# Kernel tuning notes

Measured on AMD Instinct MI355X. Metric: run time of the kernel, lower is better.

Reference implementation:

```python
import jax, jax.numpy as jnp
import numpy as np

B, H, S, D = 4, 8, 8192, 64


def setup_inputs() -> dict:
    key = jax.random.key(0)
    kq, kk, kv_, kqm, kkm = jax.random.split(key, 5)
    q = jax.random.normal(kq, (B, H, S, D), dtype=jnp.float32)
    k = jax.random.normal(kk, (B, H, S, D), dtype=jnp.float32)
    v = jax.random.normal(kv_, (B, H, S, D), dtype=jnp.float32)
    q_mask = jax.random.randint(kqm, (B, S), 0, 2).astype(jnp.bool_)
    kv_mask = jax.random.randint(kkm, (B, S), 0, 2).astype(jnp.bool_)
    return {"q": q, "k": k, "v": v, "q_mask": q_mask, "kv_mask": kv_mask}


def reference(q, k, v, q_mask, kv_mask):
    # Linear (kernelized) attention branch: feature map phi(x) = elu(x) + 1
    qe = jax.nn.elu(q) + 1.0
    ke = jax.nn.elu(k) + 1.0
    qm = q_mask.astype(q.dtype)[:, None, :, None]   # [B,1,S,1]
    km = kv_mask.astype(q.dtype)[:, None, :, None]
    qe = qe * qm
    ke = ke * km
    ve = v * km
    s = v.shape[2]
    # kv: [B,H,D,D] contraction over kv sequence
    kv = jnp.einsum('bhsd,bhsc->bhdc', ke, ve / s)
    # normalizer per query position: [B,H,L]
    div = 1.0 / (jnp.einsum('bhld,bhsd->bhl', qe, ke) + 1e-6)
    out = s * jnp.einsum('bhld,bhdc,bhl->bhlc', qe, kv, div)
    return out
```

## Files before the change

kernel.cpp:

```cpp
#include <hip/hip_runtime.h>


#define S_LEN 8192
#define NBH 32
#define KVSTRIDE 4160

typedef __attribute__((ext_vector_type(4))) float f32x4;

__device__ __forceinline__ float elu1(float x) {
  return x > 0.0f ? (x + 1.0f) : __expf(x);
}

__global__ __launch_bounds__(256) void k1_partial(
    const float* __restrict__ kin, const float* __restrict__ vin,
    const int* __restrict__ kv_mask, float* __restrict__ partials, int seg_rows) {
  __shared__ float ke_lds[64 * 64];
  __shared__ float ve_lds[64 * 64];
  const int tid = threadIdx.x;
  const int seg = blockIdx.x, bh = blockIdx.y, b = bh >> 3;
  const int rbase = seg * seg_rows;
  const int dg = tid >> 4, cg = tid & 15;
  const float* kbase = kin + (size_t)bh * S_LEN * 64;
  const float* vbase = vin + (size_t)bh * S_LEN * 64;
  const int* mbase = kv_mask + b * S_LEN;

  f32x4 ka[4], va[4], kb[4], vb[4];
  float ma[4], mb[4];
  float acc[4][4];
#pragma unroll
  for (int i = 0; i < 4; ++i)
#pragma unroll
    for (int j = 0; j < 4; ++j) acc[i][j] = 0.f;
  f32x4 ksump = {0.f, 0.f, 0.f, 0.f};

#define LOAD_T(K, V, M, r0_)                                           \
  {                                                                    \
    const float* kp_ = kbase + (size_t)(r0_) * 64;                     \
    const float* vp_ = vbase + (size_t)(r0_) * 64;                     \
    _Pragma("unroll")                                                  \
    for (int i_ = 0; i_ < 4; ++i_) {                                   \
      int f_ = tid + 256 * i_;                                         \
      K[i_] = *(const f32x4*)(kp_ + (size_t)f_ * 4);                   \
      V[i_] = *(const f32x4*)(vp_ + (size_t)f_ * 4);                   \
      M[i_] = mbase[(r0_) + (tid >> 4) + 16 * i_] ? 1.0f : 0.0f;       \
    }                                                                  \
  }

#define STORE_T(K, V, M)                                               \
  {                                                                    \
    _Pragma("unroll")                                                  \
    for (int i_ = 0; i_ < 4; ++i_) {                                   \
      int row_ = (tid >> 4) + 16 * i_;                                 \
      int c4_ = (tid & 15) * 4;                                        \
      float m_ = M[i_];                                                \
      float mv_ = m_ * (1.0f / 8192.0f);                               \
      f32x4 ke4_, ve4_;                                                \
      _Pragma("unroll")                                                \
      for (int j_ = 0; j_ < 4; ++j_) {                                 \
        ke4_[j_] = elu1(K[i_][j_]) * m_;                               \
        ve4_[j_] = V[i_][j_] * mv_;                                    \
      }                                                                \
      ksump += ke4_;      \
      *(f32x4*)&ke_lds[row_ * 64 + c4_] = ke4_;                        \
      *(f32x4*)&ve_lds[row_ * 64 + c4_] = ve4_;                        \
    }                                                                  \
  }

#define COMPUTE_T()                                                    \
  {                                                                    \
    _Pragma("unroll 4")                                                \
    for (int s_ = 0; s_ < 64; ++s_) {                                  \
      f32x4 kd_ = *(const f32x4*)&ke_lds[s_ * 64 + dg * 4];            \
      f32x4 vc_ = *(const f32x4*)&ve_lds[s_ * 64 + cg * 4];            \
      _Pragma("unroll")                                                \
      for (int i_ = 0; i_ < 4; ++i_)                                   \
        _Pragma("unroll")                                              \
        for (int j_ = 0; j_ < 4; ++j_)                                 \
          acc[i_][j_] = fmaf(kd_[i_], vc_[j_], acc[i_][j_]);           \
    }                                                                  \
  }

  const int ntiles = seg_rows >> 6;
  LOAD_T(ka, va, ma, rbase)
  for (int t = 0; t < ntiles; t += 2) {
    if (t) __syncthreads();
    STORE_T(ka, va, ma)
    LOAD_T(kb, vb, mb, rbase + (t + 1) * 64)
    __syncthreads();
    COMPUTE_T()
    __syncthreads();
    STORE_T(kb, vb, mb)
    if (t + 2 < ntiles) LOAD_T(ka, va, ma, rbase + (t + 2) * 64)
    __syncthreads();
    COMPUTE_T()
  }

  float* p = partials + ((size_t)bh * gridDim.x + seg) * KVSTRIDE;
#pragma unroll
  for (int i = 0; i < 4; ++i) {
    f32x4 o;
#pragma unroll
    for (int j = 0; j < 4; ++j) o[j] = acc[i][j];
    *(f32x4*)&p[(dg * 4 + i) * 64 + cg * 4] = o;
  }
  __syncthreads();
  *(f32x4*)&ke_lds[tid * 4] = ksump;
  __syncthreads();
  if (tid < 64) {
    float s = 0.f;
#pragma unroll
    for (int g = 0; g < 16; ++g)
      s += ke_lds[(g * 16 + (tid >> 2)) * 4 + (tid & 3)];
    p[4096 + tid] = s;
  }
#undef LOAD_T
#undef STORE_T
#undef COMPUTE_T
}

__global__ __launch_bounds__(256) void k2_reduce(
    const float* __restrict__ partials, float* __restrict__ kvg, int nchunk) {
  const int idx = blockIdx.x * 256 + threadIdx.x;
  if (idx >= NBH * KVSTRIDE) return;
  const int bh = idx / KVSTRIDE;
  const int e = idx - bh * KVSTRIDE;
  const float* p = partials + (size_t)bh * nchunk * KVSTRIDE + e;
  float s0 = 0.f, s1 = 0.f, s2 = 0.f, s3 = 0.f;
  int c = 0;
  for (; c + 4 <= nchunk; c += 4) {
    s0 += p[(size_t)(c + 0) * KVSTRIDE];
    s1 += p[(size_t)(c + 1) * KVSTRIDE];
    s2 += p[(size_t)(c + 2) * KVSTRIDE];
    s3 += p[(size_t)(c + 3) * KVSTRIDE];
  }
  for (; c < nchunk; ++c) s0 += p[(size_t)c * KVSTRIDE];
  kvg[idx] = (s0 + s1) + (s2 + s3);
}

__global__ __launch_bounds__(256) void k3_out(
    const float* __restrict__ qin, const int* __restrict__ q_mask,
    const float* __restrict__ kvg, float* __restrict__ out) {
  __shared__ float qe_lds[64 * 66];
  __shared__ float kv_lds[64 * 64];
  __shared__ float den_lds[256 * 4];
  __shared__ float inv_lds[64];
  const int tid = threadIdx.x;
  const int rb = blockIdx.x, bh = blockIdx.y, b = bh >> 3;
  const int r0 = rb * 64;
  const int lg = tid >> 4, cg = tid & 15;
  const float* kvb = kvg + (size_t)bh * KVSTRIDE;
  const f32x4 ks4 = *(const f32x4*)(kvb + 4096 + cg * 4);
  const float* qb = qin + ((size_t)bh * S_LEN + r0) * 64;

  f32x4 denp;
#pragma unroll
  for (int i = 0; i < 4; ++i) {
    int f = tid + 256 * i;
    int row = (tid >> 4) + 16 * i, c4 = cg * 4;
    float m = q_mask[b * S_LEN + r0 + row] ? 1.0f : 0.0f;
    f32x4 qw = *(const f32x4*)(qb + (size_t)f * 4);
    f32x4 qe;
#pragma unroll
    for (int j = 0; j < 4; ++j) qe[j] = elu1(qw[j]) * m;
    *(f32x4*)&qe_lds[row * 66 + c4] = qe;
    denp[i] = qe[0] * ks4[0] + qe[1] * ks4[1] + qe[2] * ks4[2] + qe[3] * ks4[3];
    *(f32x4*)&kv_lds[f * 4] = *(const f32x4*)(kvb + (size_t)f * 4);
  }
  *(f32x4*)&den_lds[tid * 4] = denp;
  __syncthreads();
  if (tid < 64) {
    float s = 0.f;
#pragma unroll
    for (int g = 0; g < 16; ++g)
      s += den_lds[((tid & 15) * 16 + g) * 4 + (tid >> 4)];
    inv_lds[tid] = 8192.0f / (s + 1e-6f);
  }

  float acc[4][4];
#pragma unroll
  for (int i = 0; i < 4; ++i)
#pragma unroll
    for (int j = 0; j < 4; ++j) acc[i][j] = 0.f;

#pragma unroll 8
  for (int d = 0; d < 64; d += 2) {
    float2 qv0 = *(const float2*)&qe_lds[(lg * 4 + 0) * 66 + d];
    float2 qv1 = *(const float2*)&qe_lds[(lg * 4 + 1) * 66 + d];
    float2 qv2 = *(const float2*)&qe_lds[(lg * 4 + 2) * 66 + d];
    float2 qv3 = *(const float2*)&qe_lds[(lg * 4 + 3) * 66 + d];
    f32x4 kv0 = *(const f32x4*)&kv_lds[d * 64 + cg * 4];
    f32x4 kv1 = *(const f32x4*)&kv_lds[(d + 1) * 64 + cg * 4];
#pragma unroll
    for (int j = 0; j < 4; ++j) {
      acc[0][j] = fmaf(qv0.x, kv0[j], fmaf(qv0.y, kv1[j], acc[0][j]));
      acc[1][j] = fmaf(qv1.x, kv0[j], fmaf(qv1.y, kv1[j], acc[1][j]));
      acc[2][j] = fmaf(qv2.x, kv0[j], fmaf(qv2.y, kv1[j], acc[2][j]));
      acc[3][j] = fmaf(qv3.x, kv0[j], fmaf(qv3.y, kv1[j], acc[3][j]));
    }
  }
  __syncthreads();
#pragma unroll
  for (int il = 0; il < 4; ++il) {
    int row = lg * 4 + il;
    float inv = inv_lds[row];
    f32x4 o;
#pragma unroll
    for (int j = 0; j < 4; ++j) o[j] = acc[il][j] * inv;
    *(f32x4*)(out + ((size_t)bh * S_LEN + r0 + row) * 64 + cg * 4) = o;
  }
}

extern "C" void kernel_launch(void* const* d_in, const int* in_sizes, int n_in,
                              void* d_out, int out_size, void* d_ws, size_t ws_size,
                              hipStream_t stream) {
  const float* q = (const float*)d_in[0];
  const float* k = (const float*)d_in[1];
  const float* v = (const float*)d_in[2];
  const int* qm = (const int*)d_in[3];
  const int* km = (const int*)d_in[4];
  float* out = (float*)d_out;

  int nchunk = 64;
  while (nchunk > 1) {
    size_t need = (size_t)NBH * nchunk * KVSTRIDE * 4 + (size_t)NBH * KVSTRIDE * 4;
    if (need <= ws_size) break;
    nchunk >>= 1;
  }
  float* partials = (float*)d_ws;
  float* kvg = partials + (size_t)NBH * nchunk * KVSTRIDE;
  int seg_rows = S_LEN / nchunk;

  k1_partial<<<dim3(nchunk, NBH), 256, 0, stream>>>(k, v, km, partials, seg_rows);
  int n_elem = NBH * KVSTRIDE;
  k2_reduce<<<dim3((n_elem + 255) / 256), 256, 0, stream>>>(partials, kvg, nchunk);
  k3_out<<<dim3(S_LEN / 64, NBH), 256, 0, stream>>>(q, qm, kvg, out);
}
```

Before: 242.9 us.

## Double-buffer LDS tiles in k1/k3, make k3 persistent, reduce chunk count

k1 now keeps two LDS buffers, so each iteration has a single barrier and the next tile's global load overlaps the current tile's FMA loop. k3 becomes a persistent kernel: each block loads kv once and walks 8 row tiles with a double-buffered qe tile. The denominator is computed inside the main d-loop instead of through a separate LDS reduction. Fewer chunks in k1 (16 instead of 64) shrink the partials traffic and k2's work. The cost is less parallelism in k1 (512 blocks) and k3 (512 blocks), which may leave CUs underfilled on a large GPU.

```diff
diff --git a/kernel.cpp b/kernel.cpp
--- a/kernel.cpp
+++ b/kernel.cpp
@@ -4,6 +4,8 @@
 #define S_LEN 8192
 #define NBH 32
 #define KVSTRIDE 4160
+#define NCHUNK 16
+#define K3_XB 16
 
 typedef __attribute__((ext_vector_type(4))) float f32x4;
 
@@ -14,8 +16,8 @@
 __global__ __launch_bounds__(256) void k1_partial(
     const float* __restrict__ kin, const float* __restrict__ vin,
     const int* __restrict__ kv_mask, float* __restrict__ partials, int seg_rows) {
-  __shared__ float ke_lds[64 * 64];
-  __shared__ float ve_lds[64 * 64];
+  __shared__ float ke_lds[2][64 * 64];
+  __shared__ float ve_lds[2][64 * 64];
   const int tid = threadIdx.x;
   const int seg = blockIdx.x, bh = blockIdx.y, b = bh >> 3;
   const int rbase = seg * seg_rows;
@@ -24,8 +26,8 @@
   const float* vbase = vin + (size_t)bh * S_LEN * 64;
   const int* mbase = kv_mask + b * S_LEN;
 
-  f32x4 ka[4], va[4], kb[4], vb[4];
-  float ma[4], mb[4];
+  f32x4 kr[4], vr[4];
+  float mr[4];
   float acc[4][4];
 #pragma unroll
   for (int i = 0; i < 4; ++i)
@@ -33,45 +35,44 @@
     for (int j = 0; j < 4; ++j) acc[i][j] = 0.f;
   f32x4 ksump = {0.f, 0.f, 0.f, 0.f};
 
-#define LOAD_T(K, V, M, r0_)                                           \
+#define LOAD_T(r0_)                                                    \
   {                                                                    \
     const float* kp_ = kbase + (size_t)(r0_) * 64;                     \
     const float* vp_ = vbase + (size_t)(r0_) * 64;                     \
     _Pragma("unroll")                                                  \
     for (int i_ = 0; i_ < 4; ++i_) {                                   \
       int f_ = tid + 256 * i_;                                         \
-      K[i_] = *(const f32x4*)(kp_ + (size_t)f_ * 4);                   \
-      V[i_] = *(const f32x4*)(vp_ + (size_t)f_ * 4);                   \
-      M[i_] = mbase[(r0_) + (tid >> 4) + 16 * i_] ? 1.0f : 0.0f;       \
-    }                                                                  \
-  }
-
-#define STORE_T(K, V, M)                                               \
-  {                                                                    \
-    _Pragma("unroll")                                                  \
-    for (int i_ = 0; i_ < 4; ++i_) {                                   \
-      int row_ = (tid >> 4) + 16 * i_;                                 \
-      int c4_ = (tid & 15) * 4;                                        \
-      float m_ = M[i_];                                                \
+      kr[i_] = *(const f32x4*)(kp_ + (size_t)f_ * 4);                  \
+      vr[i_] = *(const f32x4*)(vp_ + (size_t)f_ * 4);                  \
+      mr[i_] = mbase[(r0_) + dg + 16 * i_] ? 1.0f : 0.0f;              \
+    }                                                                  \
+  }
+
+#define STORE_T(buf_)                                                  \
+  {                                                                    \
+    _Pragma("unroll")                                                  \
+    for (int i_ = 0; i_ < 4; ++i_) {                                   \
+      int row_ = dg + 16 * i_;                                         \
+      float m_ = mr[i_];                                               \
       float mv_ = m_ * (1.0f / 8192.0f);                               \
       f32x4 ke4_, ve4_;                                                \
       _Pragma("unroll")                                                \
       for (int j_ = 0; j_ < 4; ++j_) {                                 \
-        ke4_[j_] = elu1(K[i_][j_]) * m_;                               \
-        ve4_[j_] = V[i_][j_] * mv_;                                    \
+        ke4_[j_] = elu1(kr[i_][j_]) * m_;                              \
+        ve4_[j_] = vr[i_][j_] * mv_;                                   \
       }                                                                \
-      ksump += ke4_;      \
-      *(f32x4*)&ke_lds[row_ * 64 + c4_] = ke4_;                        \
-      *(f32x4*)&ve_lds[row_ * 64 + c4_] = ve4_;                        \
-    }                                                                  \
-  }
-
-#define COMPUTE_T()                                                    \
+      ksump += ke4_;                                                   \
+      *(f32x4*)&ke_lds[buf_][row_ * 64 + cg * 4] = ke4_;               \
+      *(f32x4*)&ve_lds[buf_][row_ * 64 + cg * 4] = ve4_;               \
+    }                                                                  \
+  }
+
+#define COMPUTE_T(buf_)                                                \
   {                                                                    \
     _Pragma("unroll 4")                                                \
     for (int s_ = 0; s_ < 64; ++s_) {                                  \
-      f32x4 kd_ = *(const f32x4*)&ke_lds[s_ * 64 + dg * 4];            \
-      f32x4 vc_ = *(const f32x4*)&ve_lds[s_ * 64 + cg * 4];            \
+      f32x4 kd_ = *(const f32x4*)&ke_lds[buf_][s_ * 64 + dg * 4];      \
+      f32x4 vc_ = *(const f32x4*)&ve_lds[buf_][s_ * 64 + cg * 4];      \
       _Pragma("unroll")                                                \
       for (int i_ = 0; i_ < 4; ++i_)                                   \
         _Pragma("unroll")                                              \
@@ -81,18 +82,13 @@
   }
 
   const int ntiles = seg_rows >> 6;
-  LOAD_T(ka, va, ma, rbase)
-  for (int t = 0; t < ntiles; t += 2) {
-    if (t) __syncthreads();
-    STORE_T(ka, va, ma)
-    LOAD_T(kb, vb, mb, rbase + (t + 1) * 64)
+  LOAD_T(rbase)
+  STORE_T(0)
+  for (int t = 0; t < ntiles; ++t) {
     __syncthreads();
-    COMPUTE_T()
-    __syncthreads();
-    STORE_T(kb, vb, mb)
-    if (t + 2 < ntiles) LOAD_T(ka, va, ma, rbase + (t + 2) * 64)
-    __syncthreads();
-    COMPUTE_T()
+    if (t + 1 < ntiles) LOAD_T(rbase + (t + 1) * 64)
+    COMPUTE_T(t & 1)
+    if (t + 1 < ntiles) STORE_T((t + 1) & 1)
   }
 
   float* p = partials + ((size_t)bh * gridDim.x + seg) * KVSTRIDE;
@@ -104,13 +100,13 @@
     *(f32x4*)&p[(dg * 4 + i) * 64 + cg * 4] = o;
   }
   __syncthreads();
-  *(f32x4*)&ke_lds[tid * 4] = ksump;
+  *(f32x4*)&ke_lds[0][tid * 4] = ksump;
   __syncthreads();
   if (tid < 64) {
     float s = 0.f;
 #pragma unroll
     for (int g = 0; g < 16; ++g)
-      s += ke_lds[(g * 16 + (tid >> 2)) * 4 + (tid & 3)];
+      s += ke_lds[0][(g * 16 + (tid >> 2)) * 4 + (tid & 3)];
     p[4096 + tid] = s;
   }
 #undef LOAD_T
@@ -140,74 +136,93 @@
 __global__ __launch_bounds__(256) void k3_out(
     const float* __restrict__ qin, const int* __restrict__ q_mask,
     const float* __restrict__ kvg, float* __restrict__ out) {
-  __shared__ float qe_lds[64 * 66];
   __shared__ float kv_lds[64 * 64];
-  __shared__ float den_lds[256 * 4];
-  __shared__ float inv_lds[64];
+  __shared__ float qe_lds[2][64 * 68];
+  __shared__ float ks_lds[64];
   const int tid = threadIdx.x;
-  const int rb = blockIdx.x, bh = blockIdx.y, b = bh >> 3;
-  const int r0 = rb * 64;
+  const int xb = blockIdx.x, bh = blockIdx.y, b = bh >> 3;
   const int lg = tid >> 4, cg = tid & 15;
   const float* kvb = kvg + (size_t)bh * KVSTRIDE;
-  const f32x4 ks4 = *(const f32x4*)(kvb + 4096 + cg * 4);
-  const float* qb = qin + ((size_t)bh * S_LEN + r0) * 64;
-
-  f32x4 denp;
+  const float* qb = qin + (size_t)bh * S_LEN * 64;
+  const int* mb = q_mask + b * S_LEN;
+
 #pragma unroll
   for (int i = 0; i < 4; ++i) {
     int f = tid + 256 * i;
-    int row = (tid >> 4) + 16 * i, c4 = cg * 4;
-    float m = q_mask[b * S_LEN + r0 + row] ? 1.0f : 0.0f;
-    f32x4 qw = *(const f32x4*)(qb + (size_t)f * 4);
-    f32x4 qe;
-#pragma unroll
-    for (int j = 0; j < 4; ++j) qe[j] = elu1(qw[j]) * m;
-    *(f32x4*)&qe_lds[row * 66 + c4] = qe;
-    denp[i] = qe[0] * ks4[0] + qe[1] * ks4[1] + qe[2] * ks4[2] + qe[3] * ks4[3];
     *(f32x4*)&kv_lds[f * 4] = *(const f32x4*)(kvb + (size_t)f * 4);
   }
-  *(f32x4*)&den_lds[tid * 4] = denp;
-  __syncthreads();
-  if (tid < 64) {
-    float s = 0.f;
-#pragma unroll
-    for (int g = 0; g < 16; ++g)
-      s += den_lds[((tid & 15) * 16 + g) * 4 + (tid >> 4)];
-    inv_lds[tid] = 8192.0f / (s + 1e-6f);
-  }
-
-  float acc[4][4];
-#pragma unroll
-  for (int i = 0; i < 4; ++i)
-#pragma unroll
-    for (int j = 0; j < 4; ++j) acc[i][j] = 0.f;
-
+  if (tid < 64) ks_lds[tid] = kvb[4096 + tid];
+
+  f32x4 qr[4];
+  float mr[4];
+
+#define LOADQ(r0_)                                                     \
+  {                                                                    \
+    const float* qp_ = qb + (size_t)(r0_) * 64;                        \
+    _Pragma("unroll")                                                  \
+    for (int i_ = 0; i_ < 4; ++i_) {                                   \
+      int f_ = tid + 256 * i_;                                         \
+      qr[i_] = *(const f32x4*)(qp_ + (size_t)f_ * 4);                  \
+      mr[i_] = mb[(r0_) + lg + 16 * i_] ? 1.0f : 0.0f;                 \
+    }                                                                  \
+  }
+
+#define STOREQ(buf_)                                                   \
+  {                                                                    \
+    _Pragma("unroll")                                                  \
+    for (int i_ = 0; i_ < 4; ++i_) {                                   \
+      int row_ = lg + 16 * i_;                                         \
+      float m_ = mr[i_];                                               \
+      f32x4 qe_;                                                       \
+      _Pragma("unroll")                                                \
+      for (int j_ = 0; j_ < 4; ++j_) qe_[j_] = elu1(qr[i_][j_]) * m_;  \
+      *(f32x4*)&qe_lds[buf_][row_ * 68 + cg * 4] = qe_;                \
+    }                                                                  \
+  }
+
+  const int c0 = xb * 8;
+  LOADQ(c0 * 64)
+  STOREQ(0)
+  for (int t = 0; t < 8; ++t) {
+    __syncthreads();
+    if (t + 1 < 8) LOADQ((c0 + t + 1) * 64)
+    float acc[4][4];
+    float den[4];
+#pragma unroll
+    for (int il = 0; il < 4; ++il) {
+      den[il] = 0.f;
+#pragma unroll
+      for (int j = 0; j < 4; ++j) acc[il][j] = 0.f;
+    }
+    const float* qbuf = qe_lds[t & 1];
 #pragma unroll 8
-  for (int d = 0; d < 64; d += 2) {
-    float2 qv0 = *(const float2*)&qe_lds[(lg * 4 + 0) * 66 + d];
-    float2 qv1 = *(const float2*)&qe_lds[(lg * 4 + 1) * 66 + d];
-    float2 qv2 = *(const float2*)&qe_lds[(lg * 4 + 2) * 66 + d];
-    float2 qv3 = *(const float2*)&qe_lds[(lg * 4 + 3) * 66 + d];
-    f32x4 kv0 = *(const f32x4*)&kv_lds[d * 64 + cg * 4];
-    f32x4 kv1 = *(const f32x4*)&kv_lds[(d + 1) * 64 + cg * 4];
-#pragma unroll
-    for (int j = 0; j < 4; ++j) {
-      acc[0][j] = fmaf(qv0.x, kv0[j], fmaf(qv0.y, kv1[j], acc[0][j]));
-      acc[1][j] = fmaf(qv1.x, kv0[j], fmaf(qv1.y, kv1[j], acc[1][j]));
-      acc[2][j] = fmaf(qv2.x, kv0[j], fmaf(qv2.y, kv1[j], acc[2][j]));
-      acc[3][j] = fmaf(qv3.x, kv0[j], fmaf(qv3.y, kv1[j], acc[3][j]));
+    for (int d = 0; d < 64; d += 2) {
+      float2 ksv = *(const float2*)&ks_lds[d];
+      f32x4 kv0 = *(const f32x4*)&kv_lds[d * 64 + cg * 4];
+      f32x4 kv1 = *(const f32x4*)&kv_lds[(d + 1) * 64 + cg * 4];
+#pragma unroll
+      for (int il = 0; il < 4; ++il) {
+        float2 qv = *(const float2*)&qbuf[(lg * 4 + il) * 68 + d];
+        den[il] = fmaf(qv.x, ksv.x, fmaf(qv.y, ksv.y, den[il]));
+#pragma unroll
+        for (int j = 0; j < 4; ++j)
+          acc[il][j] = fmaf(qv.x, kv0[j], fmaf(qv.y, kv1[j], acc[il][j]));
+      }
     }
-  }
-  __syncthreads();
-#pragma unroll
-  for (int il = 0; il < 4; ++il) {
-    int row = lg * 4 + il;
-    float inv = inv_lds[row];
-    f32x4 o;
-#pragma unroll
-    for (int j = 0; j < 4; ++j) o[j] = acc[il][j] * inv;
-    *(f32x4*)(out + ((size_t)bh * S_LEN + r0 + row) * 64 + cg * 4) = o;
-  }
+    if (t + 1 < 8) STOREQ((t + 1) & 1)
+    const int r0 = (c0 + t) * 64;
+#pragma unroll
+    for (int il = 0; il < 4; ++il) {
+      float inv = 8192.0f / (den[il] + 1e-6f);
+      int row = r0 + lg * 4 + il;
+      f32x4 o;
+#pragma unroll
+      for (int j = 0; j < 4; ++j) o[j] = acc[il][j] * inv;
+      *(f32x4*)(out + ((size_t)bh * S_LEN + row) * 64 + cg * 4) = o;
+    }
+  }
+#undef LOADQ
+#undef STOREQ
 }
 
 extern "C" void kernel_launch(void* const* d_in, const int* in_sizes, int n_in,
@@ -220,7 +235,7 @@
   const int* km = (const int*)d_in[4];
   float* out = (float*)d_out;
 
-  int nchunk = 64;
+  int nchunk = NCHUNK;
   while (nchunk > 1) {
     size_t need = (size_t)NBH * nchunk * KVSTRIDE * 4 + (size_t)NBH * KVSTRIDE * 4;
     if (need <= ws_size) break;
@@ -233,5 +248,5 @@
   k1_partial<<<dim3(nchunk, NBH), 256, 0, stream>>>(k, v, km, partials, seg_rows);
   int n_elem = NBH * KVSTRIDE;
   k2_reduce<<<dim3((n_elem + 255) / 256), 256, 0, stream>>>(partials, kvg, nchunk);
-  k3_out<<<dim3(S_LEN / 64, NBH), 256, 0, stream>>>(q, qm, kvg, out);
-}
+  k3_out<<<dim3(K3_XB, NBH), 256, 0, stream>>>(q, qm, kvg, out);
+}
```

After: 267.4 us. 1.1x slower.
